# Kernel optimization log

Measured on AMD Instinct MI355X. Metric: run time of the kernel, lower is better.

Reference implementation:

```python
import jax, jax.numpy as jnp
import numpy as np

N = 50000   # nodes
E = 800000  # edges
IN = 128    # in_channels
H = 256     # hidden_channels
G = 128     # graphs in batch
NEG_SLOPE = 0.2


def _gat_conv(x, src, dst, W, a_src, a_dst, b):
    # PyG GATConv, heads=1: xp = W x; e_ij = LeakyReLU(a_src.xp_j + a_dst.xp_i);
    # softmax over incoming edges of target i; out_i = sum_j alpha_ij xp_j + b
    xp = x @ W                                   # [N, H]
    e = jax.nn.leaky_relu(xp[src] @ a_src + xp[dst] @ a_dst, NEG_SLOPE)  # [Et]
    m = jax.ops.segment_max(e, dst, num_segments=N)
    m = jnp.where(jnp.isfinite(m), m, 0.0)
    p = jnp.exp(e - m[dst])
    denom = jax.ops.segment_sum(p, dst, num_segments=N)
    alpha = p / denom[dst]
    return jax.ops.segment_sum(alpha[:, None] * xp[src], dst, num_segments=N) + b


def _gru_step_h0(x, W_ih, W_hh, b_ih, b_hh):
    # torch.nn.GRU, seq_len=1, h0=0. Gate order: r, z, n.
    gi = x @ W_ih.T + b_ih                       # [N, 3H]
    i_r, i_z, i_n = jnp.split(gi, 3, axis=-1)
    h_r, h_z, h_n = jnp.split(b_hh, 3)           # h0=0 -> hidden gates are biases
    r = jax.nn.sigmoid(i_r + h_r)
    z = jax.nn.sigmoid(i_z + h_z)
    n = jnp.tanh(i_n + r * h_n)
    return (1.0 - z) * n                         # + z * h0 (=0)


def setup_inputs() -> dict:
    key = jax.random.key(0)
    ks = jax.random.split(key, 18)
    s = 0.05
    inp = {
        "x": jax.random.normal(ks[0], (N, IN), jnp.float32),
        "edge_index": jax.random.randint(ks[1], (2, E), 0, N, dtype=jnp.int32).astype(jnp.int64),
        "batch": jnp.sort(jax.random.randint(ks[2], (N,), 0, G, dtype=jnp.int32)).astype(jnp.int64),
        # GAT layer 0 (in->H) and layer 1 (H->H)
        "W0": jax.random.normal(ks[3], (IN, H), jnp.float32) * s,
        "a_src0": jax.random.normal(ks[4], (H,), jnp.float32) * s,
        "a_dst0": jax.random.normal(ks[5], (H,), jnp.float32) * s,
        "b0": jnp.zeros((H,), jnp.float32),
        "W1": jax.random.normal(ks[6], (H, H), jnp.float32) * s,
        "a_src1": jax.random.normal(ks[7], (H,), jnp.float32) * s,
        "a_dst1": jax.random.normal(ks[8], (H,), jnp.float32) * s,
        "b1": jnp.zeros((H,), jnp.float32),
        # GRU(H, H)
        "W_ih": jax.random.normal(ks[9], (3 * H, H), jnp.float32) * s,
        "W_hh": jax.random.normal(ks[10], (3 * H, H), jnp.float32) * s,
        "b_ih": jnp.zeros((3 * H,), jnp.float32),
        "b_hh": jnp.zeros((3 * H,), jnp.float32),
        # super_node_fc
        "Wf": jax.random.normal(ks[11], (H, H), jnp.float32) * s,
        "bf": jnp.zeros((H,), jnp.float32),
    }
    return inp


def reference(x, edge_index, batch, W0, a_src0, a_dst0, b0, W1, a_src1, a_dst1, b1,
              W_ih, W_hh, b_ih, b_hh, Wf, bf):
    # add self loops (PyG GATConv default)
    loops = jnp.arange(N, dtype=edge_index.dtype)
    src = jnp.concatenate([edge_index[0], loops])
    dst = jnp.concatenate([edge_index[1], loops])

    h = jax.nn.relu(_gat_conv(x, src, dst, W0, a_src0, a_dst0, b0))  # dropout=identity (eval)
    h = jax.nn.relu(_gat_conv(h, src, dst, W1, a_src1, a_dst1, b1))

    h = _gru_step_h0(h, W_ih, W_hh, b_ih, b_hh)                      # [N, H]

    h = jax.ops.segment_sum(h, batch, num_segments=G)                # global_add_pool [G, H]
    super_node = jnp.mean(h, axis=0, keepdims=True)                  # [1, H]
    super_node = jax.nn.relu(super_node @ Wf.T + bf)
    return jnp.concatenate([h, jnp.broadcast_to(super_node, (G, H))], axis=1)  # [G, 2H]
```

## Files before the change

### kernel.cpp

```cpp
#include <hip/hip_runtime.h>
#include <hip/hip_fp16.h>
#include <math.h>

#define N_NODES 50000
#define N_PAD   50176
#define N_EDGES 800000
#define ET (N_EDGES + N_NODES)
#define IN_CH 128
#define H 256
#define G_GRAPHS 128
#define NEG_SLOPE 0.2f
#define NB 391

typedef __attribute__((ext_vector_type(8))) short short8;
typedef __attribute__((ext_vector_type(4))) float f32x4;
typedef __attribute__((ext_vector_type(2))) float f32x2;
typedef unsigned short u16;
typedef unsigned char u8;

#if __has_builtin(__builtin_amdgcn_cvt_f32_fp8) && __has_builtin(__builtin_amdgcn_cvt_pk_fp8_f32)
#define USE_FP8_BUILTINS 1
#else
#define USE_FP8_BUILTINS 0
#endif
#if USE_FP8_BUILTINS && __has_builtin(__builtin_amdgcn_cvt_pk_f32_fp8)
#define HAVE_PK_DEC 1
#else
#define HAVE_PK_DEC 0
#endif

__device__ inline u16 f2bf(float v) {
    unsigned u = __float_as_uint(v);
    unsigned r = (u + 0x7FFFu + ((u >> 16) & 1u)) >> 16;
    return (u16)r;
}
__device__ inline float bf2f(u16 v) {
    return __uint_as_float(((unsigned)v) << 16);
}

#if USE_FP8_BUILTINS
#define FP8_WSCALE 1.0f
__device__ inline unsigned fp8_pack4(float a, float b, float c, float d) {
    int v = 0;
    v = __builtin_amdgcn_cvt_pk_fp8_f32(a, b, v, false);
    v = __builtin_amdgcn_cvt_pk_fp8_f32(c, d, v, true);
    return (unsigned)v;
}
__device__ inline void fp8_dec4(unsigned rv, float& f0, float& f1, float& f2, float& f3) {
#if HAVE_PK_DEC
    f32x2 lo = __builtin_amdgcn_cvt_pk_f32_fp8((int)rv, false);
    f32x2 hi = __builtin_amdgcn_cvt_pk_f32_fp8((int)rv, true);
    f0 = lo.x; f1 = lo.y; f2 = hi.x; f3 = hi.y;
#else
    f0 = __builtin_amdgcn_cvt_f32_fp8((int)rv, 0);
    f1 = __builtin_amdgcn_cvt_f32_fp8((int)rv, 1);
    f2 = __builtin_amdgcn_cvt_f32_fp8((int)rv, 2);
    f3 = __builtin_amdgcn_cvt_f32_fp8((int)rv, 3);
#endif
}
#else
#define FP8_WSCALE 256.0f
__device__ inline u8 fp8_enc1(float f) {
    unsigned u = __float_as_uint(f);
    unsigned s = (u >> 31) << 7;
    float a = fabsf(f);
    if (a >= 448.f) return (u8)(s | 0x7E);
    unsigned bits = __float_as_uint(a);
    int exp = (int)((bits >> 23) & 255) - 127;
    unsigned m23 = bits & 0x7fffff;
    if (exp < -6) {
        int m = (int)rintf(a * 512.f);
        if (m >= 8) return (u8)(s | (1 << 3));
        return (u8)(s | m);
    }
    int e8 = exp + 7;
    unsigned m = m23 >> 20, rem = m23 & 0xFFFFF;
    if (rem > 0x80000 || (rem == 0x80000 && (m & 1))) m++;
    if (m == 8) { m = 0; e8++; }
    if (e8 > 15 || (e8 == 15 && m == 7)) return (u8)(s | 0x7E);
    return (u8)(s | (e8 << 3) | m);
}
__device__ inline unsigned fp8_pack4(float a, float b, float c, float d) {
    return (unsigned)fp8_enc1(a) | ((unsigned)fp8_enc1(b) << 8) |
           ((unsigned)fp8_enc1(c) << 16) | ((unsigned)fp8_enc1(d) << 24);
}
__device__ inline void fp8_dec4(unsigned rv, float& f0, float& f1, float& f2, float& f3) {
    unsigned hA = ((rv & 0x00800080u) << 8) | ((rv & 0x007f007fu) << 7);
    unsigned rs = rv >> 8;
    unsigned hB = ((rs & 0x00800080u) << 8) | ((rs & 0x007f007fu) << 7);
    __half2 a = *(__half2*)&hA;
    __half2 b = *(__half2*)&hB;
    f0 = __low2float(a);  f2 = __high2float(a);
    f1 = __low2float(b);  f3 = __high2float(b);
}
#endif

__device__ inline void async_cp16(const u16* g, u16* l) {
    __builtin_amdgcn_global_load_lds(
        (const __attribute__((address_space(1))) unsigned int*)g,
        (__attribute__((address_space(3))) unsigned int*)l,
        16, 0, 0);
}

__global__ __launch_bounds__(256) void bucket_hist(const int* __restrict__ ei,
                                                   int* __restrict__ gcnt) {
    __shared__ int h[NB];
    int t = threadIdx.x;
    for (int b = t; b < NB; b += 256) h[b] = 0;
    __syncthreads();
    for (int e = blockIdx.x * 256 + t; e < N_EDGES; e += gridDim.x * 256)
        atomicAdd(&h[ei[N_EDGES + e] >> 7], 1);
    __syncthreads();
    for (int b = t; b < NB; b += 256)
        if (h[b]) atomicAdd(&gcnt[b], h[b]);
}

__global__ __launch_bounds__(512) void bucket_scan(const int* __restrict__ gcnt,
                                                   int* __restrict__ off,
                                                   int* __restrict__ cur) {
    __shared__ int s[NB + 1];
    int t = threadIdx.x;
    if (t < NB) s[t] = gcnt[t];
    __syncthreads();
    if (t == 0) {
        int a = 0;
        for (int b = 0; b < NB; b++) { int c = s[b]; s[b] = a; a += c; }
        s[NB] = a;
    }
    __syncthreads();
    if (t <= NB) { off[t] = s[t]; if (t < NB) cur[t] = s[t]; }
}

#define EPT 16
__global__ __launch_bounds__(256) void bucket_scatter(const int* __restrict__ ei,
                                                      int* __restrict__ bucketCur,
                                                      int2* __restrict__ rec) {
    __shared__ int cnt[NB];
    __shared__ int base[NB];
    int t = threadIdx.x;
    for (int b = t; b < NB; b += 256) cnt[b] = 0;
    __syncthreads();
    int e0 = blockIdx.x * (256 * EPT);
    int sa[EPT], da[EPT], rk[EPT];
#pragma unroll
    for (int k = 0; k < EPT; k++) {
        int e = e0 + k * 256 + t;
        if (e < N_EDGES) {
            sa[k] = ei[e];
            da[k] = ei[N_EDGES + e];
            rk[k] = atomicAdd(&cnt[da[k] >> 7], 1);
        }
    }
    __syncthreads();
    for (int b = t; b < NB; b += 256) {
        int c = cnt[b];
        base[b] = c ? atomicAdd(&bucketCur[b], c) : 0;
    }
    __syncthreads();
#pragma unroll
    for (int k = 0; k < EPT; k++) {
        int e = e0 + k * 256 + t;
        if (e < N_EDGES) rec[base[da[k] >> 7] + rk[k]] = make_int2(sa[k], da[k]);
    }
}

__global__ __launch_bounds__(256) void build_csr(const int2* __restrict__ rec,
                                                 const int* __restrict__ off,
                                                 int* __restrict__ indptr,
                                                 int* __restrict__ eidsSrc) {
    __shared__ int cnt[128];
    __shared__ int scn[128];
    __shared__ int cur[128];
    int b = blockIdx.x, t = threadIdx.x;
    int nInB = N_NODES - b * 128;
    if (nInB > 128) nInB = 128;
    if (t < 128) cnt[t] = 0;
    __syncthreads();
    int lo = off[b], hi = off[b + 1];
    for (int i = lo + t; i < hi; i += 256) atomicAdd(&cnt[rec[i].y & 127], 1);
    __syncthreads();
    if (t < 128) scn[t] = cnt[t] + 1;
    __syncthreads();
    for (int o = 1; o < 128; o <<= 1) {
        int v = 0;
        if (t < 128 && t >= o) v = scn[t - o];
        __syncthreads();
        if (t < 128 && t >= o) scn[t] += v;
        __syncthreads();
    }
    int base = off[b] + 128 * b;
    if (t < nInB) {
        int start = base + (t ? scn[t - 1] : 0);
        int node = b * 128 + t;
        indptr[node] = start;
        eidsSrc[start] = node;
        cur[t] = start + 1;
    }
    if (b == 0 && t == 0) indptr[N_NODES] = ET;
    __syncthreads();
    for (int i = lo + t; i < hi; i += 256) {
        int2 r = rec[i];
        int pos = atomicAdd(&cur[r.y & 127], 1);
        eidsSrc[pos] = r.x;
    }
}

__global__ __launch_bounds__(256) void prep_kernel(const float* __restrict__ x,
                                                   const float* __restrict__ Wih,
                                                   const float* __restrict__ W0,
                                                   const float* __restrict__ W1,
                                                   u16* __restrict__ x_bf,
                                                   u16* __restrict__ Wih_bf,
                                                   u16* __restrict__ W0t,
                                                   u16* __restrict__ W1t) {
    int i = blockIdx.x * 256 + threadIdx.x;
    int seg = blockIdx.y;
    if (seg == 0) {
        if (i < N_NODES * IN_CH / 4) {
            float4 v = *(const float4*)&x[i * 4];
            ushort4 o = {f2bf(v.x), f2bf(v.y), f2bf(v.z), f2bf(v.w)};
            *(ushort4*)&x_bf[i * 4] = o;
        }
    } else if (seg == 1) {
        if (i < 3 * H * H / 4) {
            float4 v = *(const float4*)&Wih[i * 4];
            ushort4 o = {f2bf(v.x), f2bf(v.y), f2bf(v.z), f2bf(v.w)};
            *(ushort4*)&Wih_bf[i * 4] = o;
        }
    } else if (seg == 2) {
        if (i < IN_CH * H) {
            int k = i / H, n = i % H;
            W0t[(size_t)n * IN_CH + k] = f2bf(W0[i]);
        }
    } else {
        if (i < H * H) {
            int k = i / H, n = i % H;
            W1t[(size_t)n * H + k] = f2bf(W1[i]);
        }
    }
}

__global__ __launch_bounds__(256, 2) void gemm_wide(const u16* __restrict__ A,
                                                    const u16* __restrict__ Bt,
                                                    u16* __restrict__ C,
                                                    int M, int K, int Ntot) {
    __shared__ u16 As[128][32];
    __shared__ u16 Bs[256][32];
    int t = threadIdx.x;
    int m0 = blockIdx.x * 128;
    int n0 = blockIdx.y * 256;
    int wave = t >> 6, lane = t & 63;
    int wm = (wave >> 1) * 64, wn = (wave & 1) * 128;
    int lrow = lane & 15;
    int lq = lane >> 4;

    f32x4 acc[4][8];
#pragma unroll
    for (int i = 0; i < 4; i++)
#pragma unroll
        for (int j = 0; j < 8; j++)
            acc[i][j] = (f32x4){0.f, 0.f, 0.f, 0.f};

    int r0 = t >> 2;
    int qs = (t & 3) ^ ((t >> 3) & 3);
    const u16* gA0 = A + (size_t)(m0 + r0) * K + qs * 8;
    const u16* gA1 = gA0 + (size_t)64 * K;
    const u16* gB0 = Bt + (size_t)(n0 + r0) * K + qs * 8;
    const u16* gB1 = gB0 + (size_t)64 * K;
    const u16* gB2 = gB0 + (size_t)128 * K;
    const u16* gB3 = gB0 + (size_t)192 * K;
    u16* lA0 = &As[0][0] + t * 8;
    u16* lA1 = lA0 + 256 * 8;
    u16* lB0 = &Bs[0][0] + t * 8;
    u16* lB1 = lB0 + 256 * 8;
    u16* lB2 = lB0 + 512 * 8;
    u16* lB3 = lB0 + 768 * 8;

    int swz8 = (lq ^ ((lrow >> 1) & 3)) * 8;

    for (int k0 = 0; k0 < K; k0 += 32) {
        __syncthreads();
        async_cp16(gA0 + k0, lA0);
        async_cp16(gA1 + k0, lA1);
        async_cp16(gB0 + k0, lB0);
        async_cp16(gB1 + k0, lB1);
        async_cp16(gB2 + k0, lB2);
        async_cp16(gB3 + k0, lB3);
        __syncthreads();
        short8 af[4], bfr[8];
#pragma unroll
        for (int i = 0; i < 4; i++)
            af[i] = *(const short8*)&As[wm + i * 16 + lrow][swz8];
#pragma unroll
        for (int j = 0; j < 8; j++)
            bfr[j] = *(const short8*)&Bs[wn + j * 16 + lrow][swz8];
#pragma unroll
        for (int i = 0; i < 4; i++)
#pragma unroll
            for (int j = 0; j < 8; j++)
                acc[i][j] = __builtin_amdgcn_mfma_f32_16x16x32_bf16(af[i], bfr[j], acc[i][j], 0, 0, 0);
    }
#pragma unroll
    for (int i = 0; i < 4; i++) {
#pragma unroll
        for (int reg = 0; reg < 4; reg++) {
            int gm = m0 + wm + i * 16 + lq * 4 + reg;
            if (gm < M) {
#pragma unroll
                for (int j = 0; j < 8; j++) {
                    int gn = n0 + wn + j * 16 + lrow;
                    C[(size_t)gm * Ntot + gn] = f2bf(acc[i][j][reg]);
                }
            }
        }
    }
}

__global__ __launch_bounds__(256) void sdot_fp8(const u16* __restrict__ xp,
                                                const float* __restrict__ a_src,
                                                const float* __restrict__ a_dst,
                                                float* __restrict__ s_src,
                                                float* __restrict__ s_dst,
                                                u8* __restrict__ xp8) {
    int wave = threadIdx.x >> 6, lane = threadIdx.x & 63;
    int n = blockIdx.x * 4 + wave;
    int col = lane << 2;
    ushort4 v = *(const ushort4*)&xp[(size_t)n * H + col];
    float4 a1 = *(const float4*)&a_src[col];
    float4 a2 = *(const float4*)&a_dst[col];
    float x0 = bf2f(v.x), x1 = bf2f(v.y), x2 = bf2f(v.z), x3 = bf2f(v.w);
    *(unsigned*)&xp8[(size_t)n * H + col] = fp8_pack4(x0, x1, x2, x3);
    float d1 = x0 * a1.x + x1 * a1.y + x2 * a1.z + x3 * a1.w;
    float d2 = x0 * a2.x + x1 * a2.y + x2 * a2.z + x3 * a2.w;
#pragma unroll
    for (int off = 32; off; off >>= 1) {
        d1 += __shfl_xor(d1, off);
        d2 += __shfl_xor(d2, off);
    }
    if (lane == 0) { s_src[n] = d1; s_dst[n] = d2; }
}

__global__ __launch_bounds__(256) void gat_agg_fp8(const u8* __restrict__ xp8,
                                                   const float* __restrict__ s_src,
                                                   const float* __restrict__ s_dst,
                                                   const int* __restrict__ indptr,
                                                   const int* __restrict__ eidsSrc,
                                                   const float* __restrict__ bias,
                                                   u16* __restrict__ out) {
    __shared__ int2 sSW[4][64];
    int wave = threadIdx.x >> 6, lane = threadIdx.x & 63;
    int n = blockIdx.x * 4 + wave;
    int start = indptr[n];
    int deg = indptr[n + 1] - start;
    float sdn = s_dst[n];
    int col = lane << 2;
    float a0 = 0.f, a1 = 0.f, a2 = 0.f, a3 = 0.f;

    if (deg <= 64) {
        int s = 0;
        float v = -1e30f;
        if (lane < deg) {
            s = eidsSrc[start + lane];
            float u = s_src[s] + sdn;
            v = (u >= 0.f) ? u : NEG_SLOPE * u;
        }
        float m = v;
#pragma unroll
        for (int off = 32; off; off >>= 1) m = fmaxf(m, __shfl_xor(m, off));
        float pw = (lane < deg) ? expf(v - m) : 0.f;
        float dsum = pw;
#pragma unroll
        for (int off = 32; off; off >>= 1) dsum += __shfl_xor(dsum, off);
        float w = pw * (FP8_WSCALE / dsum);
        sSW[wave][lane] = make_int2(s * H, __float_as_int(w));
        int j = 0;
        for (; j + 16 <= deg; j += 16) {
            unsigned rv[16];
            float wv[16];
#pragma unroll
            for (int k = 0; k < 16; k++) {
                int2 sw = sSW[wave][j + k];
                wv[k] = __int_as_float(sw.y);
                rv[k] = *(const unsigned*)&xp8[(size_t)(unsigned)sw.x + col];
            }
#pragma unroll
            for (int k = 0; k < 16; k++) {
                float f0, f1, f2, f3;
                fp8_dec4(rv[k], f0, f1, f2, f3);
                a0 += wv[k] * f0; a1 += wv[k] * f1;
                a2 += wv[k] * f2; a3 += wv[k] * f3;
            }
        }
        if (j + 8 <= deg) {
            unsigned rv[8];
            float wv[8];
#pragma unroll
            for (int k = 0; k < 8; k++) {
                int2 sw = sSW[wave][j + k];
                wv[k] = __int_as_float(sw.y);
                rv[k] = *(const unsigned*)&xp8[(size_t)(unsigned)sw.x + col];
            }
#pragma unroll
            for (int k = 0; k < 8; k++) {
                float f0, f1, f2, f3;
                fp8_dec4(rv[k], f0, f1, f2, f3);
                a0 += wv[k] * f0; a1 += wv[k] * f1;
                a2 += wv[k] * f2; a3 += wv[k] * f3;
            }
            j += 8;
        }
        for (; j < deg; j++) {
            int2 sw = sSW[wave][j];
            float wj = __int_as_float(sw.y);
            unsigned rv = *(const unsigned*)&xp8[(size_t)(unsigned)sw.x + col];
            float f0, f1, f2, f3;
            fp8_dec4(rv, f0, f1, f2, f3);
            a0 += wj * f0; a1 += wj * f1; a2 += wj * f2; a3 += wj * f3;
        }
    } else {
        float m = -1e30f;
        for (int i = lane; i < deg; i += 64) {
            int s = eidsSrc[start + i];
            float u = s_src[s] + sdn;
            u = (u >= 0.f) ? u : NEG_SLOPE * u;
            m = fmaxf(m, u);
        }
#pragma unroll
        for (int off = 32; off; off >>= 1) m = fmaxf(m, __shfl_xor(m, off));
        float dsum = 0.f;
        for (int i = lane; i < deg; i += 64) {
            int s = eidsSrc[start + i];
            float u = s_src[s] + sdn;
            u = (u >= 0.f) ? u : NEG_SLOPE * u;
            dsum += expf(u - m);
        }
#pragma unroll
        for (int off = 32; off; off >>= 1) dsum += __shfl_xor(dsum, off);
        float dinv = FP8_WSCALE / dsum;
        for (int base = 0; base < deg; base += 64) {
            int cnt = min(64, deg - base);
            int s = 0; float w = 0.f;
            if (lane < cnt) {
                s = eidsSrc[start + base + lane];
                float u = s_src[s] + sdn;
                u = (u >= 0.f) ? u : NEG_SLOPE * u;
                w = expf(u - m) * dinv;
            }
            sSW[wave][lane] = make_int2(s * H, __float_as_int(w));
            for (int j = 0; j < cnt; j++) {
                int2 sw = sSW[wave][j];
                float wj = __int_as_float(sw.y);
                unsigned rv = *(const unsigned*)&xp8[(size_t)(unsigned)sw.x + col];
                float f0, f1, f2, f3;
                fp8_dec4(rv, f0, f1, f2, f3);
                a0 += wj * f0; a1 += wj * f1; a2 += wj * f2; a3 += wj * f3;
            }
        }
    }
    float4 bv = *(const float4*)&bias[col];
    ushort4 o;
    o.x = f2bf(fmaxf(a0 + bv.x, 0.f));
    o.y = f2bf(fmaxf(a1 + bv.y, 0.f));
    o.z = f2bf(fmaxf(a2 + bv.z, 0.f));
    o.w = f2bf(fmaxf(a3 + bv.w, 0.f));
    *(ushort4*)&out[(size_t)n * H + col] = o;
}

__global__ __launch_bounds__(256) void gru_gates_pool(const u16* __restrict__ gates,
                                                      const float* __restrict__ b_ih,
                                                      const float* __restrict__ b_hh,
                                                      const int* __restrict__ batch,
                                                      float* __restrict__ pooled) {
    int t = threadIdx.x;
    int i0 = blockIdx.x * 16;
    if (i0 >= N_NODES) return;
    float bir = b_ih[t], biz = b_ih[256 + t], bin_ = b_ih[512 + t];
    float bhr = b_hh[t], bhz = b_hh[256 + t], bhn = b_hh[512 + t];
    int iend = min(16, N_NODES - i0);
    float acc = 0.f;
    int cur_g = batch[i0];
    for (int i = 0; i < iend; i++) {
        size_t row = (size_t)(i0 + i) * 768;
        float ir = bf2f(gates[row + t]);
        float iz = bf2f(gates[row + 256 + t]);
        float in_ = bf2f(gates[row + 512 + t]);
        float r = 1.f / (1.f + expf(-(ir + bir + bhr)));
        float z = 1.f / (1.f + expf(-(iz + biz + bhz)));
        float nn = tanhf(in_ + bin_ + r * bhn);
        float h = (1.f - z) * nn;
        int g = batch[i0 + i];
        if (g != cur_g) {
            atomicAdd(&pooled[(size_t)cur_g * H + t], acc);
            acc = 0.f;
            cur_g = g;
        }
        acc += h;
    }
    atomicAdd(&pooled[(size_t)cur_g * H + t], acc);
}

__global__ __launch_bounds__(256) void super_kernel(const float* __restrict__ pooled,
                                                    const float* __restrict__ Wf,
                                                    const float* __restrict__ bf,
                                                    float* __restrict__ sup) {
    __shared__ float smean[256];
    int t = threadIdx.x;
    float s = 0.f;
    for (int g = 0; g < G_GRAPHS; g++) s += pooled[(size_t)g * H + t];
    smean[t] = s / (float)G_GRAPHS;
    __syncthreads();
    float acc = 0.f;
    for (int k = 0; k < H; k++) acc += smean[k] * Wf[(size_t)t * H + k];
    acc += bf[t];
    sup[t] = fmaxf(acc, 0.f);
}

__global__ __launch_bounds__(256) void writeout(const float* __restrict__ pooled,
                                                const float* __restrict__ sup,
                                                float* __restrict__ out) {
    int idx = blockIdx.x * 256 + threadIdx.x;
    int g = idx >> 9, c = idx & 511;
    out[idx] = (c < H) ? pooled[(size_t)g * H + c] : sup[c - H];
}

extern "C" void kernel_launch(void* const* d_in, const int* in_sizes, int n_in,
                              void* d_out, int out_size, void* d_ws, size_t ws_size,
                              hipStream_t stream) {
    const float* x      = (const float*)d_in[0];
    const int*   ei     = (const int*)d_in[1];
    const int*   batch  = (const int*)d_in[2];
    const float* W0     = (const float*)d_in[3];
    const float* a_src0 = (const float*)d_in[4];
    const float* a_dst0 = (const float*)d_in[5];
    const float* b0     = (const float*)d_in[6];
    const float* W1     = (const float*)d_in[7];
    const float* a_src1 = (const float*)d_in[8];
    const float* a_dst1 = (const float*)d_in[9];
    const float* b1     = (const float*)d_in[10];
    const float* W_ih   = (const float*)d_in[11];
    const float* b_ih   = (const float*)d_in[13];
    const float* b_hh   = (const float*)d_in[14];
    const float* Wf     = (const float*)d_in[15];
    const float* bf     = (const float*)d_in[16];
    float* out = (float*)d_out;

    char* p = (char*)d_ws;
    auto alloc = [&](size_t bytes) -> void* {
        void* r = (void*)p;
        p += (bytes + 255) & ~(size_t)255;
        return r;
    };
    u16*   xp_bf  = (u16*)alloc((size_t)N_PAD * H * 2);
    u16*   h_bf   = (u16*)alloc((size_t)N_PAD * H * 2);
    u16*   x_bf   = (u16*)alloc((size_t)N_PAD * IN_CH * 2);
    u8*    xp8    = (u8*)x_bf;
    u16*   gatesC = (u16*)alloc((size_t)N_PAD * 3 * H * 2);
    u16*   W0t    = (u16*)alloc((size_t)H * IN_CH * 2);
    u16*   W1t    = (u16*)alloc((size_t)H * H * 2);
    u16*   Wih_bf = (u16*)alloc((size_t)3 * H * H * 2);
    float* s_src  = (float*)alloc((size_t)N_NODES * 4);
    float* s_dst  = (float*)alloc((size_t)N_NODES * 4);
    int2*  rec    = (int2*)alloc((size_t)N_EDGES * 8);
    int*   eidsSrc= (int*)alloc((size_t)ET * 4);
    int*   indptr = (int*)alloc((size_t)(N_NODES + 1) * 4);
    int*   gBkt   = (int*)alloc((size_t)(NB + 1) * 4);
    int*   bktOff = (int*)alloc((size_t)(NB + 1) * 4);
    int*   bktCur = (int*)alloc((size_t)(NB + 1) * 4);
    float* pooled = (float*)alloc((size_t)G_GRAPHS * H * 4);
    float* sup    = (float*)alloc((size_t)H * 4);

    hipMemsetAsync(gBkt, 0, (size_t)NB * 4, stream);
    bucket_hist<<<NB, 256, 0, stream>>>(ei, gBkt);
    bucket_scan<<<1, 512, 0, stream>>>(gBkt, bktOff, bktCur);
    bucket_scatter<<<(N_EDGES + 256 * EPT - 1) / (256 * EPT), 256, 0, stream>>>(ei, bktCur, rec);
    build_csr<<<NB, 256, 0, stream>>>(rec, bktOff, indptr, eidsSrc);

    prep_kernel<<<dim3((N_NODES * IN_CH / 4 + 255) / 256, 4), 256, 0, stream>>>(
        x, W_ih, W0, W1, x_bf, Wih_bf, W0t, W1t);

    const int MB = (N_NODES + 127) / 128;
    const int WB = N_NODES / 4;
    gemm_wide<<<dim3(MB, 1), 256, 0, stream>>>(x_bf, W0t, xp_bf, N_NODES, IN_CH, H);
    sdot_fp8<<<WB, 256, 0, stream>>>(xp_bf, a_src0, a_dst0, s_src, s_dst, xp8);
    gat_agg_fp8<<<WB, 256, 0, stream>>>(xp8, s_src, s_dst, indptr, eidsSrc, b0, h_bf);
    gemm_wide<<<dim3(MB, 1), 256, 0, stream>>>(h_bf, W1t, xp_bf, N_NODES, H, H);
    sdot_fp8<<<WB, 256, 0, stream>>>(xp_bf, a_src1, a_dst1, s_src, s_dst, xp8);
    gat_agg_fp8<<<WB, 256, 0, stream>>>(xp8, s_src, s_dst, indptr, eidsSrc, b1, h_bf);
    hipMemsetAsync(pooled, 0, (size_t)G_GRAPHS * H * 4, stream);
    gemm_wide<<<dim3(MB, 3), 256, 0, stream>>>(h_bf, Wih_bf, gatesC, N_NODES, H, 3 * H);
    gru_gates_pool<<<(N_NODES + 15) / 16, 256, 0, stream>>>(gatesC, b_ih, b_hh, batch, pooled);
    super_kernel<<<1, 256, 0, stream>>>(pooled, Wf, bf, sup);
    writeout<<<(G_GRAPHS * 2 * H) / 256, 256, 0, stream>>>(pooled, sup, out);
}
```

Before: 356.1 us.

## Fuse attention dot products and FP8 packing into GAT GEMM epilogue

```diff
diff --git a/kernel.cpp b/kernel.cpp
--- a/kernel.cpp
+++ b/kernel.cpp
@@ -17,6 +17,7 @@
 typedef __attribute__((ext_vector_type(2))) float f32x2;
 typedef unsigned short u16;
 typedef unsigned char u8;
+
 
 #if __has_builtin(__builtin_amdgcn_cvt_f32_fp8) && __has_builtin(__builtin_amdgcn_cvt_pk_fp8_f32)
 #define USE_FP8_BUILTINS 1
@@ -209,10 +210,14 @@
                                                    const float* __restrict__ Wih,
                                                    const float* __restrict__ W0,
                                                    const float* __restrict__ W1,
+                                                   const float* __restrict__ b0,
+                                                   const float* __restrict__ b1,
                                                    u16* __restrict__ x_bf,
                                                    u16* __restrict__ Wih_bf,
                                                    u16* __restrict__ W0t,
-                                                   u16* __restrict__ W1t) {
+                                                   u16* __restrict__ W1t,
+                                                   float* __restrict__ b0p,
+                                                   float* __restrict__ b1p) {
     int i = blockIdx.x * 256 + threadIdx.x;
     int seg = blockIdx.y;
     if (seg == 0) {
@@ -222,30 +227,45 @@
             *(ushort4*)&x_bf[i * 4] = o;
         }
     } else if (seg == 1) {
-        if (i < 3 * H * H / 4) {
-            float4 v = *(const float4*)&Wih[i * 4];
-            ushort4 o = {f2bf(v.x), f2bf(v.y), f2bf(v.z), f2bf(v.w)};
-            *(ushort4*)&Wih_bf[i * 4] = o;
+        if (i < 3 * H * H) {
+            int r = i >> 8, p = i & 255;
+            int c = ((p & 15) << 4) | (p >> 4);
+            Wih_bf[(size_t)r * H + p] = f2bf(Wih[(size_t)r * H + c]);
         }
     } else if (seg == 2) {
         if (i < IN_CH * H) {
             int k = i / H, n = i % H;
             W0t[(size_t)n * IN_CH + k] = f2bf(W0[i]);
         }
+    } else if (seg == 3) {
+        if (i < H * H) {
+            int n = i >> 8, p = i & 255;
+            int c = ((p & 15) << 4) | (p >> 4);
+            W1t[(size_t)n * H + p] = f2bf(W1[(size_t)c * H + n]);
+        }
     } else {
-        if (i < H * H) {
-            int k = i / H, n = i % H;
-            W1t[(size_t)n * H + k] = f2bf(W1[i]);
-        }
-    }
-}
-
+        if (i < H) {
+            int c = ((i & 15) << 4) | (i >> 4);
+            b0p[i] = b0[c];
+            b1p[i] = b1[c];
+        }
+    }
+}
+
+template <bool FUSE>
 __global__ __launch_bounds__(256, 2) void gemm_wide(const u16* __restrict__ A,
                                                     const u16* __restrict__ Bt,
                                                     u16* __restrict__ C,
+                                                    u8* __restrict__ C8,
+                                                    const float* __restrict__ avS,
+                                                    const float* __restrict__ avD,
+                                                    float* __restrict__ sS,
+                                                    float* __restrict__ sD,
                                                     int M, int K, int Ntot) {
     __shared__ u16 As[128][32];
     __shared__ u16 Bs[256][32];
+    __shared__ float rSp[2][128];
+    __shared__ float rDp[2][128];
     int t = threadIdx.x;
     int m0 = blockIdx.x * 128;
     int n0 = blockIdx.y * 256;
@@ -300,44 +320,67 @@
             for (int j = 0; j < 8; j++)
                 acc[i][j] = __builtin_amdgcn_mfma_f32_16x16x32_bf16(af[i], bfr[j], acc[i][j], 0, 0, 0);
     }
-#pragma unroll
-    for (int i = 0; i < 4; i++) {
-#pragma unroll
-        for (int reg = 0; reg < 4; reg++) {
-            int gm = m0 + wm + i * 16 + lq * 4 + reg;
+
+    if constexpr (FUSE) {
+        float aS[8], aD[8];
+#pragma unroll
+        for (int j = 0; j < 8; j++) {
+            aS[j] = avS[wn + j * 16 + lrow];
+            aD[j] = avD[wn + j * 16 + lrow];
+        }
+        int woff = wn ? 8 : 0;
+#pragma unroll
+        for (int i = 0; i < 4; i++) {
+#pragma unroll
+            for (int reg = 0; reg < 4; reg++) {
+                float ps = 0.f, pd = 0.f;
+#pragma unroll
+                for (int j = 0; j < 8; j++) {
+                    float v = acc[i][j][reg];
+                    ps += v * aS[j];
+                    pd += v * aD[j];
+                }
+                uint2 pk;
+                pk.x = fp8_pack4(acc[i][0][reg], acc[i][1][reg], acc[i][2][reg], acc[i][3][reg]);
+                pk.y = fp8_pack4(acc[i][4][reg], acc[i][5][reg], acc[i][6][reg], acc[i][7][reg]);
+                int row = m0 + wm + i * 16 + lq * 4 + reg;
+                *(uint2*)&C8[(size_t)row * 256 + lrow * 16 + woff] = pk;
+#pragma unroll
+                for (int msk = 1; msk < 16; msk <<= 1) {
+                    ps += __shfl_xor(ps, msk);
+                    pd += __shfl_xor(pd, msk);
+                }
+                if (lrow == 0) {
+                    int lr = wm + i * 16 + lq * 4 + reg;
+                    rSp[wave & 1][lr] = ps;
+                    rDp[wave & 1][lr] = pd;
+                }
+            }
+        }
+        __syncthreads();
+        if (t < 128) {
+            int gm = m0 + t;
             if (gm < M) {
-#pragma unroll
-                for (int j = 0; j < 8; j++) {
-                    int gn = n0 + wn + j * 16 + lrow;
-                    C[(size_t)gm * Ntot + gn] = f2bf(acc[i][j][reg]);
+                sS[gm] = rSp[0][t] + rSp[1][t];
+                sD[gm] = rDp[0][t] + rDp[1][t];
+            }
+        }
+    } else {
+#pragma unroll
+        for (int i = 0; i < 4; i++) {
+#pragma unroll
+            for (int reg = 0; reg < 4; reg++) {
+                int gm = m0 + wm + i * 16 + lq * 4 + reg;
+                if (gm < M) {
+#pragma unroll
+                    for (int j = 0; j < 8; j++) {
+                        int gn = n0 + wn + j * 16 + lrow;
+                        C[(size_t)gm * Ntot + gn] = f2bf(acc[i][j][reg]);
+                    }
                 }
             }
         }
     }
-}
-
-__global__ __launch_bounds__(256) void sdot_fp8(const u16* __restrict__ xp,
-                                                const float* __restrict__ a_src,
-                                                const float* __restrict__ a_dst,
-                                                float* __restrict__ s_src,
-                                                float* __restrict__ s_dst,
-                                                u8* __restrict__ xp8) {
-    int wave = threadIdx.x >> 6, lane = threadIdx.x & 63;
-    int n = blockIdx.x * 4 + wave;
-    int col = lane << 2;
-    ushort4 v = *(const ushort4*)&xp[(size_t)n * H + col];
-    float4 a1 = *(const float4*)&a_src[col];
-    float4 a2 = *(const float4*)&a_dst[col];
-    float x0 = bf2f(v.x), x1 = bf2f(v.y), x2 = bf2f(v.z), x3 = bf2f(v.w);
-    *(unsigned*)&xp8[(size_t)n * H + col] = fp8_pack4(x0, x1, x2, x3);
-    float d1 = x0 * a1.x + x1 * a1.y + x2 * a1.z + x3 * a1.w;
-    float d2 = x0 * a2.x + x1 * a2.y + x2 * a2.z + x3 * a2.w;
-#pragma unroll
-    for (int off = 32; off; off >>= 1) {
-        d1 += __shfl_xor(d1, off);
-        d2 += __shfl_xor(d2, off);
-    }
-    if (lane == 0) { s_src[n] = d1; s_dst[n] = d2; }
 }
 
 __global__ __launch_bounds__(256) void gat_agg_fp8(const u8* __restrict__ xp8,
@@ -550,14 +593,15 @@
         p += (bytes + 255) & ~(size_t)255;
         return r;
     };
-    u16*   xp_bf  = (u16*)alloc((size_t)N_PAD * H * 2);
     u16*   h_bf   = (u16*)alloc((size_t)N_PAD * H * 2);
     u16*   x_bf   = (u16*)alloc((size_t)N_PAD * IN_CH * 2);
-    u8*    xp8    = (u8*)x_bf;
+    u8*    xp8    = (u8*)alloc((size_t)N_PAD * H);
     u16*   gatesC = (u16*)alloc((size_t)N_PAD * 3 * H * 2);
     u16*   W0t    = (u16*)alloc((size_t)H * IN_CH * 2);
     u16*   W1t    = (u16*)alloc((size_t)H * H * 2);
     u16*   Wih_bf = (u16*)alloc((size_t)3 * H * H * 2);
+    float* b0p    = (float*)alloc((size_t)H * 4);
+    float* b1p    = (float*)alloc((size_t)H * 4);
     float* s_src  = (float*)alloc((size_t)N_NODES * 4);
     float* s_dst  = (float*)alloc((size_t)N_NODES * 4);
     int2*  rec    = (int2*)alloc((size_t)N_EDGES * 8);
@@ -575,19 +619,20 @@
     bucket_scatter<<<(N_EDGES + 256 * EPT - 1) / (256 * EPT), 256, 0, stream>>>(ei, bktCur, rec);
     build_csr<<<NB, 256, 0, stream>>>(rec, bktOff, indptr, eidsSrc);
 
-    prep_kernel<<<dim3((N_NODES * IN_CH / 4 + 255) / 256, 4), 256, 0, stream>>>(
-        x, W_ih, W0, W1, x_bf, Wih_bf, W0t, W1t);
+    prep_kernel<<<dim3((N_NODES * IN_CH / 4 + 255) / 256, 5), 256, 0, stream>>>(
+        x, W_ih, W0, W1, b0, b1, x_bf, Wih_bf, W0t, W1t, b0p, b1p);
 
     const int MB = (N_NODES + 127) / 128;
     const int WB = N_NODES / 4;
-    gemm_wide<<<dim3(MB, 1), 256, 0, stream>>>(x_bf, W0t, xp_bf, N_NODES, IN_CH, H);
-    sdot_fp8<<<WB, 256, 0, stream>>>(xp_bf, a_src0, a_dst0, s_src, s_dst, xp8);
-    gat_agg_fp8<<<WB, 256, 0, stream>>>(xp8, s_src, s_dst, indptr, eidsSrc, b0, h_bf);
-    gemm_wide<<<dim3(MB, 1), 256, 0, stream>>>(h_bf, W1t, xp_bf, N_NODES, H, H);
-    sdot_fp8<<<WB, 256, 0, stream>>>(xp_bf, a_src1, a_dst1, s_src, s_dst, xp8);
-    gat_agg_fp8<<<WB, 256, 0, stream>>>(xp8, s_src, s_dst, indptr, eidsSrc, b1, h_bf);
+    gemm_wide<true><<<dim3(MB, 1), 256, 0, stream>>>(
+        x_bf, W0t, nullptr, xp8, a_src0, a_dst0, s_src, s_dst, N_NODES, IN_CH, H);
+    gat_agg_fp8<<<WB, 256, 0, stream>>>(xp8, s_src, s_dst, indptr, eidsSrc, b0p, h_bf);
+    gemm_wide<true><<<dim3(MB, 1), 256, 0, stream>>>(
+        h_bf, W1t, nullptr, xp8, a_src1, a_dst1, s_src, s_dst, N_NODES, H, H);
+    gat_agg_fp8<<<WB, 256, 0, stream>>>(xp8, s_src, s_dst, indptr, eidsSrc, b1p, h_bf);
     hipMemsetAsync(pooled, 0, (size_t)G_GRAPHS * H * 4, stream);
-    gemm_wide<<<dim3(MB, 3), 256, 0, stream>>>(h_bf, Wih_bf, gatesC, N_NODES, H, 3 * H);
+    gemm_wide<false><<<dim3(MB, 3), 256, 0, stream>>>(
+        h_bf, Wih_bf, gatesC, nullptr, nullptr, nullptr, nullptr, nullptr, N_NODES, H, 3 * H);
     gru_gates_pool<<<(N_NODES + 15) / 16, 256, 0, stream>>>(gatesC, b_ih, b_hh, batch, pooled);
     super_kernel<<<1, 256, 0, stream>>>(pooled, Wf, bf, sup);
     writeout<<<(G_GRAPHS * 2 * H) / 256, 256, 0, stream>>>(pooled, sup, out);
```

After: 337.9 us, median of 2. -5.1%, faster.
